# Kernel tuning notes

Measured on AMD Instinct MI355X. Metric: run time of the kernel, lower is better.

The kernel has to match this reference:

```python
import jax, jax.numpy as jnp
import numpy as np

B, CIN, COUT, L, K, HEADS, GROUPS, EPS = 16, 256, 512, 1024, 3, 8, 32, 1e-5


def group_norm(x, w, b, groups, eps=EPS):
    Bx, C, Lx = x.shape
    g = x.reshape(Bx, groups, C // groups, Lx)
    mu = g.mean(axis=(2, 3), keepdims=True)
    var = g.var(axis=(2, 3), keepdims=True)
    g = (g - mu) * jax.lax.rsqrt(var + eps)
    return g.reshape(Bx, C, Lx) * w[None, :, None] + b[None, :, None]


def conv1d(x, w, b, pad):
    y = jax.lax.conv_general_dilated(x, w, window_strides=(1,), padding=[(pad, pad)],
                                     dimension_numbers=('NCH', 'OIH', 'NCH'))
    return y + b[None, :, None]


def setup_inputs() -> dict:
    key = jax.random.key(0)
    ks = jax.random.split(key, 12)
    def kn(k, shape, fan_in, scale=1.0):
        return (np.sqrt(1.0 / fan_in) * jax.random.normal(k, shape, dtype=jnp.float32)) * scale
    return {
        'x': jax.random.normal(ks[0], (B, CIN, L), dtype=jnp.float32),
        'norm0_w': jnp.ones((CIN,), jnp.float32), 'norm0_b': jnp.zeros((CIN,), jnp.float32),
        'conv0_w': kn(ks[1], (COUT, CIN, K), CIN * K), 'conv0_b': jnp.zeros((COUT,), jnp.float32),
        'norm1_w': jnp.ones((COUT,), jnp.float32), 'norm1_b': jnp.zeros((COUT,), jnp.float32),
        'conv1_w': kn(ks[2], (COUT, COUT, K), COUT * K, 1e-5), 'conv1_b': jnp.zeros((COUT,), jnp.float32),
        'skip_w': kn(ks[3], (COUT, CIN, 1), CIN), 'skip_b': jnp.zeros((COUT,), jnp.float32),
        'norm2_w': jnp.ones((COUT,), jnp.float32), 'norm2_b': jnp.zeros((COUT,), jnp.float32),
        'qkv_w': kn(ks[4], (COUT * 3, COUT, 1), COUT), 'qkv_b': jnp.zeros((COUT * 3,), jnp.float32),
        'proj_w': kn(ks[5], (COUT, COUT, 1), COUT, 1e-5), 'proj_b': jnp.zeros((COUT,), jnp.float32),
    }


def reference(x, norm0_w, norm0_b, conv0_w, conv0_b, norm1_w, norm1_b, conv1_w, conv1_b,
              skip_w, skip_b, norm2_w, norm2_b, qkv_w, qkv_b, proj_w, proj_b):
    orig = x
    h = conv1d(jax.nn.silu(group_norm(x, norm0_w, norm0_b, min(GROUPS, CIN))), conv0_w, conv0_b, (K - 1) // 2)
    h = jax.nn.silu(group_norm(h, norm1_w, norm1_b, min(GROUPS, COUT)))
    h = conv1d(h, conv1_w, conv1_b, (K - 1) // 2)
    h = h + conv1d(orig, skip_w, skip_b, 0)  # skip (in != out), dropout p=0
    # skip_scale = 1
    # attention: qkv [B, 3C, L] -> [B*H, C/H, 3, L] (channel axis splits as H, C/H, 3)
    qkv = conv1d(group_norm(h, norm2_w, norm2_b, min(GROUPS, COUT)), qkv_w, qkv_b, 0)
    ch = COUT // HEADS
    qkv = qkv.reshape(B * HEADS, ch, 3, L)
    q, k, v = qkv[:, :, 0], qkv[:, :, 1], qkv[:, :, 2]  # each [BH, ch, L]
    scores = jnp.einsum('nci,ncj->nij', q, k) / np.sqrt(ch).astype(np.float32)
    attn = jax.nn.softmax(scores, axis=-1)
    a = jnp.einsum('nij,ncj->nci', attn, v).reshape(B, COUT, L)
    return h + conv1d(a, proj_w, proj_b, 0)
```

## Files before the change

### kernel.cpp

```cpp
#include <hip/hip_runtime.h>


typedef float f32x4 __attribute__((ext_vector_type(4)));
typedef float f32x16 __attribute__((ext_vector_type(16)));
typedef short short8 __attribute__((ext_vector_type(8)));

__device__ __forceinline__ unsigned short f2bf(float f) {
  union { float f; unsigned u; } v; v.f = f;
  return (unsigned short)((v.u + 0x7FFFu + ((v.u >> 16) & 1u)) >> 16);
}
__device__ __forceinline__ float bf2f(unsigned short h) {
  union { unsigned u; float f; } v; v.u = ((unsigned)h) << 16;
  return v.f;
}

__device__ __forceinline__ float fexp2(float x) {
  float r;
  asm("v_exp_f32 %0, %1" : "=v"(r) : "v"(x));
  return r;
}

__device__ __forceinline__ void gload_lds16(const void* g, void* l) {
  __builtin_amdgcn_global_load_lds(
      (const __attribute__((address_space(1))) unsigned int*)g,
      (__attribute__((address_space(3))) unsigned int*)l, 16, 0, 0);
}

__device__ __forceinline__ float swap_add(float x) {
  float a = x, b = x;
  asm("v_permlane32_swap_b32 %0, %1" : "+v"(a), "+v"(b));
  return a + b;
}

__device__ __forceinline__ short8 pack8(float a0, float a1, float a2, float a3,
                                        float a4, float a5, float a6, float a7) {
  unsigned x0, x1, x2, x3;
  asm("v_cvt_pk_bf16_f32 %0, %1, %2" : "=v"(x0) : "v"(a0), "v"(a1));
  asm("v_cvt_pk_bf16_f32 %0, %1, %2" : "=v"(x1) : "v"(a2), "v"(a3));
  asm("v_cvt_pk_bf16_f32 %0, %1, %2" : "=v"(x2) : "v"(a4), "v"(a5));
  asm("v_cvt_pk_bf16_f32 %0, %1, %2" : "=v"(x3) : "v"(a6), "v"(a7));
  asm("v_permlane32_swap_b32 %0, %1" : "+v"(x0), "+v"(x2));
  asm("v_permlane32_swap_b32 %0, %1" : "+v"(x1), "+v"(x3));
  union { unsigned u[4]; short8 s; } r;
  r.u[0] = x0; r.u[1] = x1; r.u[2] = x2; r.u[3] = x3;
  return r.s;
}
#define PACK8(V, B) pack8(V[B+0], V[B+1], V[B+2], V[B+3], V[B+4], V[B+5], V[B+6], V[B+7])

__global__ __launch_bounds__(256) void prep_stats(
    const float* __restrict__ c0w, const float* __restrict__ c1w,
    const float* __restrict__ skw, const float* __restrict__ qw,
    const float* __restrict__ pw,
    unsigned short* __restrict__ WT0, unsigned short* __restrict__ WT1,
    unsigned short* __restrict__ WSK, unsigned short* __restrict__ WQ,
    unsigned short* __restrict__ WP,
    const float* __restrict__ x, float2* __restrict__ mr,
    unsigned short* __restrict__ outT) {
  __shared__ float2 red[4];
  const int t = threadIdx.x;
  if (blockIdx.x >= 9216) {
    const int blk = blockIdx.x - 9216;
    const int g = blk & 31;
    const int bb = blk >> 5;
    const size_t base = ((size_t)bb * 256 + g * 8) * 1024;
    float s = 0.f, ss = 0.f;
#pragma unroll
    for (int i = t * 4; i < 8192; i += 1024) {
      const float4 v = *(const float4*)(x + base + i);
      s += (v.x + v.y) + (v.z + v.w);
      ss += (v.x * v.x + v.y * v.y) + (v.z * v.z + v.w * v.w);
    }
#pragma unroll
    for (int off = 32; off; off >>= 1) {
      s += __shfl_down(s, off);
      ss += __shfl_down(ss, off);
    }
    if ((t & 63) == 0) red[t >> 6] = make_float2(s, ss);
    __syncthreads();
    const float2 r0 = red[0], r1 = red[1], r2 = red[2], r3 = red[3];
    const float tots = (r0.x + r1.x) + (r2.x + r3.x);
    const float totss = (r0.y + r1.y) + (r2.y + r3.y);
    const float mean = tots * (1.f / 8192.f);
    const float var = totss * (1.f / 8192.f) - mean * mean;
    if (t == 0) mr[bb * 32 + g] = make_float2(mean, rsqrtf(var + 1e-5f));
    unsigned short* ob = outT + (size_t)bb * 1026 * 256 + g * 8;
    if (t < 8) {
      ob[t] = 0;
      ob[(size_t)1025 * 256 + t] = 0;
    }
    return;
  }
  int idx = blockIdx.x * 256 + t;
  if (idx < 393216) {
    const int ci = idx & 255; const int rem = idx >> 8;
    const int co = rem & 511; const int kk = rem >> 9;
    WT0[idx] = f2bf(c0w[((size_t)co * 256 + ci) * 3 + kk]); return;
  }
  idx -= 393216;
  if (idx < 786432) {
    const int ci = idx & 511; const int rem = idx >> 9;
    const int co = rem & 511; const int kk = rem >> 9;
    WT1[idx] = f2bf(c1w[((size_t)co * 512 + ci) * 3 + kk]); return;
  }
  idx -= 786432;
  if (idx < 131072) { WSK[idx] = f2bf(skw[idx]); return; }
  idx -= 131072;
  if (idx < 786432) {
    const int ci = idx & 511; const int m = idx >> 9;
    const int s = m >> 9, rem = m & 511, h = rem >> 6, c = rem & 63;
    WQ[idx] = f2bf(qw[((size_t)(h * 192 + c * 3 + s) * 512) + ci]); return;
  }
  idx -= 786432;
  WP[idx] = f2bf(pw[idx]);
}

template<int MODE, bool SILU, int C, bool PADZ, bool RAW, bool IN16>
__global__ __launch_bounds__(256) void nt_kernel(
    const float* __restrict__ in, const float2* __restrict__ st,
    const float* __restrict__ gw, const float* __restrict__ gb,
    unsigned short* __restrict__ outT, unsigned short* __restrict__ rawT) {
  constexpr int CPG = C / 32;
  __shared__ float ls[64][65];
  __shared__ unsigned short lsr[RAW ? 64 : 1][72];
  __shared__ float2 gstat[4];
  const int b = blockIdx.z, c0 = blockIdx.y * 64, l0 = blockIdx.x * 64;
  const int t = threadIdx.x;
  if (MODE == 2) {
    if (t < 4) {
      const int g = (c0 >> 4) + t;
      const float2* p = st + (((size_t)b * 4 + (g >> 3)) * 8 + (g & 7)) * 8;
      float s = 0.f, ss = 0.f;
#pragma unroll
      for (int i = 0; i < 8; ++i) { s += p[i].x; ss += p[i].y; }
      const float mean = s * (1.f / 16384.f);
      const float var = ss * (1.f / 16384.f) - mean * mean;
      gstat[t] = make_float2(mean, rsqrtf(var + 1e-5f));
    }
    __syncthreads();
  }
  const int lw = (t & 15) * 4;
  const int cr = t >> 4;
#pragma unroll
  for (int p = 0; p < 4; ++p) {
    const int c = p * 16 + cr;
    const int cc = c0 + c;
    float sc = 1.f, bi = 0.f;
    if (MODE == 1) {
      const float2 ms = st[b * 32 + cc / CPG];
      sc = gw[cc] * ms.y;
      bi = gb[cc] - ms.x * sc;
    } else if (MODE == 2) {
      const float2 ms = gstat[c >> 4];
      sc = gw[cc] * ms.y;
      bi = gb[cc] - ms.x * sc;
    }
    float4 v;
    if (IN16) {
      const ushort4 u4 = *(const ushort4*)((const unsigned short*)in +
                                           ((size_t)b * C + cc) * 1024 + l0 + lw);
      v = make_float4(bf2f(u4.x), bf2f(u4.y), bf2f(u4.z), bf2f(u4.w));
    } else {
      v = *(const float4*)(in + ((size_t)b * C + cc) * 1024 + l0 + lw);
    }
    if (RAW) {
      lsr[c][lw + 0] = f2bf(v.x);
      lsr[c][lw + 1] = f2bf(v.y);
      lsr[c][lw + 2] = f2bf(v.z);
      lsr[c][lw + 3] = f2bf(v.w);
    }
    float o[4] = {v.x * sc + bi, v.y * sc + bi, v.z * sc + bi, v.w * sc + bi};
    if (SILU) {
#pragma unroll
      for (int d = 0; d < 4; ++d) o[d] = o[d] / (1.f + __expf(-o[d]));
    }
#pragma unroll
    for (int d = 0; d < 4; ++d) ls[c][lw + d] = o[d];
  }
  __syncthreads();
  const int l = t >> 2, c16 = (t & 3) * 16;
  short8 v0, v1;
#pragma unroll
  for (int j = 0; j < 8; ++j) v0[j] = (short)f2bf(ls[c16 + j][l]);
#pragma unroll
  for (int j = 0; j < 8; ++j) v1[j] = (short)f2bf(ls[c16 + 8 + j][l]);
  unsigned short* ob = outT + ((size_t)b * 1026 + l0 + l + 1) * C + c0 + c16;
  *(short8*)ob = v0;
  *(short8*)(ob + 8) = v1;
  if (RAW) {
    short8 w0, w1;
#pragma unroll
    for (int j = 0; j < 8; ++j) w0[j] = (short)lsr[c16 + j][l];
#pragma unroll
    for (int j = 0; j < 8; ++j) w1[j] = (short)lsr[c16 + 8 + j][l];
    unsigned short* rb = rawT + ((size_t)b * 1026 + l0 + l + 1) * C + c0 + c16;
    *(short8*)rb = w0;
    *(short8*)(rb + 8) = w1;
  }
  if (PADZ) {
    const short8 z = {};
    if (blockIdx.x == 0 && t < 8)
      *(short8*)(outT + (size_t)b * 1026 * C + c0 + t * 8) = z;
    if (blockIdx.x == 15 && t < 8)
      *(short8*)(outT + ((size_t)b * 1026 + 1025) * C + c0 + t * 8) = z;
  }
}

__global__ __launch_bounds__(256) void ntE_kernel(
    const unsigned short* __restrict__ Ht, const float2* __restrict__ part,
    const float* __restrict__ gw, const float* __restrict__ gb,
    unsigned short* __restrict__ outT) {
  __shared__ float2 gstat[32];
  const int b = blockIdx.y;
  const int t = threadIdx.x;
  if (t < 32) {
    const float2* p = part + (((size_t)b * 4 + (t >> 3)) * 8 + (t & 7)) * 8;
    float s = 0.f, ss = 0.f;
#pragma unroll
    for (int i = 0; i < 8; ++i) { s += p[i].x; ss += p[i].y; }
    const float mean = s * (1.f / 16384.f);
    const float var = ss * (1.f / 16384.f) - mean * mean;
    gstat[t] = make_float2(mean, rsqrtf(var + 1e-5f));
  }
  __syncthreads();
  const int c8 = t & 63;
  const float2 ms = gstat[c8 >> 1];
  const int cbase = c8 * 8;
  const float4 g0 = *(const float4*)(gw + cbase);
  const float4 g1 = *(const float4*)(gw + cbase + 4);
  const float4 b0 = *(const float4*)(gb + cbase);
  const float4 b1 = *(const float4*)(gb + cbase + 4);
  float sc[8], bi[8];
  sc[0] = g0.x * ms.y; sc[1] = g0.y * ms.y; sc[2] = g0.z * ms.y; sc[3] = g0.w * ms.y;
  sc[4] = g1.x * ms.y; sc[5] = g1.y * ms.y; sc[6] = g1.z * ms.y; sc[7] = g1.w * ms.y;
  bi[0] = b0.x - ms.x * sc[0]; bi[1] = b0.y - ms.x * sc[1];
  bi[2] = b0.z - ms.x * sc[2]; bi[3] = b0.w - ms.x * sc[3];
  bi[4] = b1.x - ms.x * sc[4]; bi[5] = b1.y - ms.x * sc[5];
  bi[6] = b1.z - ms.x * sc[6]; bi[7] = b1.w - ms.x * sc[7];
#pragma unroll
  for (int pass = 0; pass < 4; ++pass) {
    const int lp = blockIdx.x * 16 + pass * 4 + (t >> 6) + 1;
    const size_t o = ((size_t)b * 1026 + lp) * 512 + cbase;
    const short8 v = *(const short8*)(Ht + o);
    short8 r;
#pragma unroll
    for (int e = 0; e < 8; ++e) {
      const float y = bf2f((unsigned short)v[e]) * sc[e] + bi[e];
      r[e] = (short)f2bf(y / (1.f + __expf(-y)));
    }
    *(short8*)(outT + o) = r;
  }
  const short8 z = {};
  if (blockIdx.x == 0 && t < 64)
    *(short8*)(outT + (size_t)b * 1026 * 512 + t * 8) = z;
  if (blockIdx.x == 63 && t < 64)
    *(short8*)(outT + ((size_t)b * 1026 + 1025) * 512 + t * 8) = z;
}

template<int K, bool ADD, bool SCATTER, bool FUSE, bool STATS, bool TROUT,
         bool OUT16, bool ADD16>
__global__ __launch_bounds__(256, 2) void convmm_kernel(
    const unsigned short* __restrict__ Xt, const unsigned short* __restrict__ Wt,
    const float* __restrict__ bias, const float* __restrict__ addsrc,
    float* __restrict__ outp,
    unsigned short* __restrict__ qd, unsigned short* __restrict__ kd,
    unsigned short* __restrict__ vd, int Cin, int Cout,
    const unsigned short* __restrict__ X2, const unsigned short* __restrict__ W2,
    const float* __restrict__ bias2, int Cin2, float2* __restrict__ part) {
  constexpr int XR = (K == 3) ? 160 : 128;
  __shared__ __align__(16) unsigned short smem[K * 128 * 64 + XR * 64];
  unsigned short* wT = smem;
  unsigned short* xT = smem + K * 128 * 64;
  const int t = threadIdx.x, lane = t & 63, w = t >> 6;
  const int b = blockIdx.z, co0 = blockIdx.y * 128, l0 = blockIdx.x * 128;
  const int m0 = (w >> 1) * 64, n0 = (w & 1) * 64;
  const int START = (K == 3) ? l0 : (l0 + 1);
  f32x4 acc[4][4] = {};
  for (int ci0 = 0; ci0 < Cin; ci0 += 64) {
    __syncthreads();
    for (int rr = 0; rr < K * 4; ++rr) {
      const int row = rr * 32 + (t >> 3);
      const int co = row & 127;
      const int c16 = (t & 7) ^ (co & 7);
      gload_lds16(Wt + ((size_t)(row >> 7) * Cout + co0 + co) * Cin + ci0 + c16 * 8,
                  (char*)wT + (rr * 256 + t) * 16);
    }
    for (int rr = 0; rr < XR / 32; ++rr) {
      const int r = rr * 32 + (t >> 3);
      int lp = START + r;
      if (lp > 1025) lp = 1025;
      const int c16 = (t & 7) ^ (r & 7);
      gload_lds16(Xt + ((size_t)b * 1026 + lp) * Cin + ci0 + c16 * 8,
                  (char*)xT + (rr * 256 + t) * 16);
    }
    __syncthreads();
#pragma unroll
    for (int kk = 0; kk < K; ++kk) {
#pragma unroll
      for (int ks = 0; ks < 2; ++ks) {
        short8 af[4], bfr[4];
#pragma unroll
        for (int mf = 0; mf < 4; ++mf) {
          const int row = m0 + mf * 16 + (lane & 15);
          const int u = (kk * 128 + row) * 8 + ((ks * 4 + (lane >> 4)) ^ (row & 7));
          af[mf] = *(const short8*)(wT + u * 8);
        }
#pragma unroll
        for (int nf = 0; nf < 4; ++nf) {
          const int r = n0 + nf * 16 + (lane & 15) + kk;
          const int u = r * 8 + ((ks * 4 + (lane >> 4)) ^ (r & 7));
          bfr[nf] = *(const short8*)(xT + u * 8);
        }
#pragma unroll
        for (int mf = 0; mf < 4; ++mf)
#pragma unroll
          for (int nf = 0; nf < 4; ++nf)
            acc[mf][nf] = __builtin_amdgcn_mfma_f32_16x16x32_bf16(
                af[mf], bfr[nf], acc[mf][nf], 0, 0, 0);
      }
    }
  }
  if (FUSE) {
    for (int ci0 = 0; ci0 < Cin2; ci0 += 64) {
      __syncthreads();
      for (int rr = 0; rr < 4; ++rr) {
        const int co = rr * 32 + (t >> 3);
        const int c16 = (t & 7) ^ (co & 7);
        gload_lds16(W2 + (size_t)(co0 + co) * Cin2 + ci0 + c16 * 8,
                    (char*)wT + (rr * 256 + t) * 16);
      }
      for (int rr = 0; rr < 4; ++rr) {
        const int r = rr * 32 + (t >> 3);
        const int lp = l0 + 1 + r;
        const int c16 = (t & 7) ^ (r & 7);
        gload_lds16(X2 + ((size_t)b * 1026 + lp) * Cin2 + ci0 + c16 * 8,
                    (char*)xT + (rr * 256 + t) * 16);
      }
      __syncthreads();
#pragma unroll
      for (int ks = 0; ks < 2; ++ks) {
        short8 af[4], bfr[4];
#pragma unroll
        for (int mf = 0; mf < 4; ++mf) {
          const int row = m0 + mf * 16 + (lane & 15);
          const int u = row * 8 + ((ks * 4 + (lane >> 4)) ^ (row & 7));
          af[mf] = *(const short8*)(wT + u * 8);
        }
#pragma unroll
        for (int nf = 0; nf < 4; ++nf) {
          const int r = n0 + nf * 16 + (lane & 15);
          const int u = r * 8 + ((ks * 4 + (lane >> 4)) ^ (r & 7));
          bfr[nf] = *(const short8*)(xT + u * 8);
        }
#pragma unroll
        for (int mf = 0; mf < 4; ++mf)
#pragma unroll
          for (int nf = 0; nf < 4; ++nf)
            acc[mf][nf] = __builtin_amdgcn_mfma_f32_16x16x32_bf16(
                af[mf], bfr[nf], acc[mf][nf], 0, 0, 0);
      }
    }
  }
  if (TROUT) {
    __syncthreads();
    unsigned short* TP = smem;
    float2* sr = (float2*)(TP + 128 * 128);
    float sg[4] = {}, ssg[4] = {};
#pragma unroll
    for (int mf = 0; mf < 4; ++mf)
#pragma unroll
      for (int r = 0; r < 4; ++r) {
        const int mloc = m0 + mf * 16 + (lane >> 4) * 4 + r;
        const float bv = bias[co0 + mloc];
#pragma unroll
        for (int nf = 0; nf < 4; ++nf) {
          const int l = n0 + nf * 16 + (lane & 15);
          const float v = acc[mf][nf][r] + bv;
          sg[mf] += v; ssg[mf] += v * v;
          const int u = l * 16 + ((mloc >> 3) ^ (l & 7));
          TP[u * 8 + (mloc & 7)] = f2bf(v);
        }
      }
#pragma unroll
    for (int mf = 0; mf < 4; ++mf) {
      float s = sg[mf], ss = ssg[mf];
#pragma unroll
      for (int off = 32; off; off >>= 1) {
        s += __shfl_down(s, off);
        ss += __shfl_down(ss, off);
      }
      if (lane == 0)
        sr[(((w >> 1) * 4 + mf) << 1) | (w & 1)] = make_float2(s, ss);
    }
    __syncthreads();
    for (int it = 0; it < 8; ++it) {
      const int idx = it * 256 + t;
      const int l = idx >> 4, mu = idx & 15;
      const short8 v = *(const short8*)(TP + (l * 16 + (mu ^ (l & 7))) * 8);
      *(short8*)(qd + ((size_t)b * 1026 + l0 + l + 1) * 512 + co0 + mu * 8) = v;
    }
    if (t < 8) {
      const float2 a = sr[t * 2], c = sr[t * 2 + 1];
      part[(((size_t)b * 4 + blockIdx.y) * 8 + t) * 8 + blockIdx.x] =
          make_float2(a.x + c.x, a.y + c.y);
    }
  } else if (!SCATTER) {
    float sg[4] = {}, ssg[4] = {};
#pragma unroll
    for (int mf = 0; mf < 4; ++mf) {
#pragma unroll
      for (int r = 0; r < 4; ++r) {
        const int co = co0 + m0 + mf * 16 + (lane >> 4) * 4 + r;
        float bv = bias[co];
        if (FUSE) bv += bias2[co];
#pragma unroll
        for (int nf = 0; nf < 4; ++nf) {
          const int l = l0 + n0 + nf * 16 + (lane & 15);
          const size_t o = ((size_t)b * Cout + co) * 1024 + l;
          float v = acc[mf][nf][r] + bv;
          if (ADD) {
            if (ADD16) v += bf2f(((const unsigned short*)addsrc)[o]);
            else       v += addsrc[o];
          }
          if (OUT16) ((unsigned short*)outp)[o] = f2bf(v);
          else       outp[o] = v;
          if (STATS) { sg[mf] += v; ssg[mf] += v * v; }
        }
      }
    }
    if (STATS) {
      __syncthreads();
      float2* sr = (float2*)smem;
#pragma unroll
      for (int mf = 0; mf < 4; ++mf) {
        float s = sg[mf], ss = ssg[mf];
#pragma unroll
        for (int off = 32; off; off >>= 1) {
          s += __shfl_down(s, off);
          ss += __shfl_down(ss, off);
        }
        if (lane == 0)
          sr[(((w >> 1) * 4 + mf) << 1) | (w & 1)] = make_float2(s, ss);
      }
      __syncthreads();
      if (t < 8) {
        const float2 a = sr[t * 2], c = sr[t * 2 + 1];
        part[(((size_t)b * 4 + blockIdx.y) * 8 + t) * 8 + blockIdx.x] =
            make_float2(a.x + c.x, a.y + c.y);
      }
    }
  } else {
    __syncthreads();
    unsigned short* TP = smem;
    const int sidx = co0 >> 9;
    const int mbase = co0 & 511;
    const float qscale = (sidx == 0) ? 0.18033688f : 1.0f;
    if (sidx < 2) {
#pragma unroll
      for (int mf = 0; mf < 4; ++mf)
#pragma unroll
        for (int r = 0; r < 4; ++r) {
          const int mloc = m0 + mf * 16 + (lane >> 4) * 4 + r;
          const int mg = mbase + mloc;
          const float bv = bias[(mg >> 6) * 192 + (mg & 63) * 3 + sidx];
#pragma unroll
          for (int nf = 0; nf < 4; ++nf) {
            const int l = n0 + nf * 16 + (lane & 15);
            const int u = l * 16 + ((mloc >> 3) ^ (l & 7));
            TP[u * 8 + (mloc & 7)] = f2bf((acc[mf][nf][r] + bv) * qscale);
          }
        }
      __syncthreads();
      unsigned short* dst = (sidx == 0) ? qd : kd;
      for (int it = 0; it < 8; ++it) {
        const int idx = it * 256 + t;
        const int l = idx >> 4, mu = idx & 15;
        const int mg = mbase + mu * 8;
        const int bh = b * 8 + (mg >> 6);
        const short8 v = *(const short8*)(TP + (l * 16 + (mu ^ (l & 7))) * 8);
        *(short8*)(dst + ((size_t)bh * 1024 + l0 + l) * 64 + (mg & 63)) = v;
      }
    } else {
#pragma unroll
      for (int mf = 0; mf < 4; ++mf)
#pragma unroll
        for (int r = 0; r < 4; ++r) {
          const int mloc = m0 + mf * 16 + (lane >> 4) * 4 + r;
          const int mg = mbase + mloc;
          const float bv = bias[(mg >> 6) * 192 + (mg & 63) * 3 + 2];
#pragma unroll
          for (int nf = 0; nf < 4; ++nf) {
            const int l = n0 + nf * 16 + (lane & 15);
            const int u = mloc * 16 + ((l >> 3) ^ ((mloc & 7) << 1));
            TP[u * 8 + (l & 7)] = f2bf(acc[mf][nf][r] + bv);
          }
        }
      __syncthreads();
      for (int it = 0; it < 8; ++it) {
        const int idx = it * 256 + t;
        const int mloc = idx >> 4, lu = idx & 15;
        const int mg = mbase + mloc;
        const int bh = b * 8 + (mg >> 6);
        const short8 v =
            *(const short8*)(TP + (mloc * 16 + (lu ^ ((mloc & 7) << 1))) * 8);
        *(short8*)(vd + ((size_t)bh * 64 + (mg & 63)) * 1024 + l0 + lu * 8) = v;
      }
    }
  }
}

__global__ __launch_bounds__(256, 4) void attn_mfma(
    const unsigned short* __restrict__ Qb, const unsigned short* __restrict__ Kb,
    const unsigned short* __restrict__ Vb, unsigned short* __restrict__ Ab) {
  __shared__ __align__(16) unsigned short Ks[2][64 * 64];
  __shared__ __align__(16) unsigned short Vs[2][64 * 64];
  unsigned short* QP = &Ks[0][0];
  const int t = threadIdx.x, lane = t & 63, w = t >> 6;
  const int hi = lane >> 5, l31 = lane & 31;
  const int id = blockIdx.x;
  const int slot = id >> 3;
  const int bh = ((id & 7) << 4) | (slot >> 3);
  const int b = bh >> 3, h = bh & 7;
  const int iq0 = (slot & 7) * 128;
  const unsigned short* Qg = Qb + ((size_t)bh * 1024 + iq0) * 64;
  const unsigned short* Kg = Kb + (size_t)bh * 1024 * 64;
  const unsigned short* Vg = Vb + (size_t)bh * 64 * 1024;
  for (int rr = 0; rr < 4; ++rr) {
    const int r = rr * 32 + (t >> 3), c16 = (t & 7) ^ (r & 7);
    gload_lds16(Qg + (size_t)r * 64 + c16 * 8, (char*)QP + (rr * 256 + t) * 16);
  }
  __syncthreads();
  const int irow = w * 32 + l31;
  short8 qf[4];
#pragma unroll
  for (int kc = 0; kc < 4; ++kc) {
    const int u = irow * 8 + ((kc * 2 + hi) ^ (irow & 7));
    qf[kc] = *(const short8*)(QP + u * 8);
  }
  __syncthreads();
  for (int rr = 0; rr < 2; ++rr) {
    const int r = rr * 32 + (t >> 3), c16 = (t & 7) ^ (r & 7);
    gload_lds16(Kg + (size_t)r * 64 + c16 * 8, (char*)Ks[0] + (rr * 256 + t) * 16);
    gload_lds16(Vg + (size_t)r * 1024 + c16 * 8, (char*)Vs[0] + (rr * 256 + t) * 16);
  }
  __syncthreads();
  float lsum = 0.f;
  f32x16 oA[2] = {};
  auto kv_iter = [&](const int ti, const int cur) {
    if (ti < 15) {
      const int j1 = (ti + 1) * 64;
      for (int rr = 0; rr < 2; ++rr) {
        const int r = rr * 32 + (t >> 3), c16 = (t & 7) ^ (r & 7);
        gload_lds16(Kg + (size_t)(j1 + r) * 64 + c16 * 8,
                    (char*)Ks[cur ^ 1] + (rr * 256 + t) * 16);
        gload_lds16(Vg + (size_t)r * 1024 + j1 + c16 * 8,
                    (char*)Vs[cur ^ 1] + (rr * 256 + t) * 16);
      }
    }
    f32x16 sA0 = {}, sA1 = {};
    __builtin_amdgcn_s_setprio(1);
#pragma unroll
    for (int kc = 0; kc < 4; ++kc) {
      const int r0 = l31, r1 = 32 + l31;
      const short8 k0 = *(const short8*)(Ks[cur] + (r0 * 8 + ((kc * 2 + hi) ^ (r0 & 7))) * 8);
      const short8 k1 = *(const short8*)(Ks[cur] + (r1 * 8 + ((kc * 2 + hi) ^ (r1 & 7))) * 8);
      sA0 = __builtin_amdgcn_mfma_f32_32x32x16_bf16(k0, qf[kc], sA0, 0, 0, 0);
      sA1 = __builtin_amdgcn_mfma_f32_32x32x16_bf16(k1, qf[kc], sA1, 0, 0, 0);
    }
    __builtin_amdgcn_s_setprio(0);
    float p0 = 0.f, p1 = 0.f, p2 = 0.f, p3 = 0.f;
#pragma unroll
    for (int r = 0; r < 16; r += 4) {
      sA0[r + 0] = fexp2(sA0[r + 0]); p0 += sA0[r + 0];
      sA0[r + 1] = fexp2(sA0[r + 1]); p1 += sA0[r + 1];
      sA0[r + 2] = fexp2(sA0[r + 2]); p2 += sA0[r + 2];
      sA0[r + 3] = fexp2(sA0[r + 3]); p3 += sA0[r + 3];
    }
#pragma unroll
    for (int r = 0; r < 16; r += 4) {
      sA1[r + 0] = fexp2(sA1[r + 0]); p0 += sA1[r + 0];
      sA1[r + 1] = fexp2(sA1[r + 1]); p1 += sA1[r + 1];
      sA1[r + 2] = fexp2(sA1[r + 2]); p2 += sA1[r + 2];
      sA1[r + 3] = fexp2(sA1[r + 3]); p3 += sA1[r + 3];
    }
    lsum += (p0 + p1) + (p2 + p3);
    short8 pb[4];
    pb[0] = PACK8(sA0, 0);
    pb[1] = PACK8(sA0, 8);
    pb[2] = PACK8(sA1, 0);
    pb[3] = PACK8(sA1, 8);
    __builtin_amdgcn_s_setprio(1);
#pragma unroll
    for (int cf = 0; cf < 2; ++cf) {
      const int row = cf * 32 + l31;
#pragma unroll
      for (int s = 0; s < 4; ++s) {
        const int u = row * 8 + ((s * 2 + hi) ^ (row & 7));
        const short8 va = *(const short8*)(Vs[cur] + u * 8);
        oA[cf] = __builtin_amdgcn_mfma_f32_32x32x16_bf16(va, pb[s], oA[cf], 0, 0, 0);
      }
    }
    __builtin_amdgcn_s_setprio(0);
    __syncthreads();
  };
  for (int ti = 0; ti < 16; ti += 2) {
    kv_iter(ti, 0);
    kv_iter(ti + 1, 1);
  }
  const float inv = 1.f / swap_add(lsum);
#pragma unroll
  for (int cf = 0; cf < 2; ++cf)
#pragma unroll
    for (int r = 0; r < 16; ++r) {
      const int c = cf * 32 + (r & 3) + 8 * (r >> 2) + 4 * hi;
      const int u = irow * 8 + ((c >> 3) ^ (irow & 7));
      QP[u * 8 + (c & 7)] = f2bf(oA[cf][r] * inv);
    }
  for (int rr = 0; rr < 4; ++rr) {
    const int row = w * 32 + rr * 8 + (lane >> 3);
    const int c16 = lane & 7;
    const int u = row * 8 + (c16 ^ (row & 7));
    const short8 vv = *(const short8*)(QP + u * 8);
    *(short8*)(Ab + ((size_t)b * 1026 + iq0 + row + 1) * 512 + h * 64 + c16 * 8) = vv;
  }
}

#define MB(x) ((size_t)(x) << 20)

extern "C" void kernel_launch(void* const* d_in, const int* in_sizes, int n_in,
                              void* d_out, int out_size, void* d_ws,
                              size_t ws_size, hipStream_t stream) {
  const float* x   = (const float*)d_in[0];
  const float* n0w = (const float*)d_in[1];
  const float* n0b = (const float*)d_in[2];
  const float* c0w = (const float*)d_in[3];
  const float* c0b = (const float*)d_in[4];
  const float* n1w = (const float*)d_in[5];
  const float* n1b = (const float*)d_in[6];
  const float* c1w = (const float*)d_in[7];
  const float* c1b = (const float*)d_in[8];
  const float* skw = (const float*)d_in[9];
  const float* skb = (const float*)d_in[10];
  const float* n2w = (const float*)d_in[11];
  const float* n2b = (const float*)d_in[12];
  const float* qw  = (const float*)d_in[13];
  const float* qb  = (const float*)d_in[14];
  const float* pw  = (const float*)d_in[15];
  const float* pb  = (const float*)d_in[16];
  char* wsb = (char*)d_ws;
  unsigned short* WT0 = (unsigned short*)(wsb);
  unsigned short* WT1 = (unsigned short*)(wsb + MB(1));
  unsigned short* WSK = (unsigned short*)(wsb + MB(3));
  unsigned short* WQ  = (unsigned short*)(wsb + MB(4));
  unsigned short* WP  = (unsigned short*)(wsb + MB(6));
  unsigned short* H2b = (unsigned short*)(wsb + MB(7));
  unsigned short* Qb2 = (unsigned short*)(wsb + MB(41));
  unsigned short* Kb2 = (unsigned short*)(wsb + MB(58));
  unsigned short* H0t = (unsigned short*)(wsb + MB(75));
  unsigned short* Vb2 = (unsigned short*)(wsb + MB(75));
  unsigned short* Xt2 = (unsigned short*)(wsb + MB(92));
  unsigned short* Xt0 = (unsigned short*)(wsb + MB(109));
  unsigned short* Xt1 = (unsigned short*)(wsb + MB(109));
  unsigned short* Ab  = (unsigned short*)(wsb + MB(109));
  unsigned short* Xbf = (unsigned short*)(wsb + MB(126));
  float2* MR0   = (float2*)(wsb + MB(135));
  float2* PART1 = (float2*)(wsb + MB(135) + 8192);
  float2* PART2 = (float2*)(wsb + MB(135) + 32768);
  float* outp = (float*)d_out;

  prep_stats<<<9728, 256, 0, stream>>>(c0w, c1w, skw, qw, pw,
                                       WT0, WT1, WSK, WQ, WP, x, MR0, Xt0);
  nt_kernel<1, true, 256, false, true, false><<<dim3(16, 4, 16), 256, 0, stream>>>(
      x, MR0, n0w, n0b, Xt0, Xbf);
  convmm_kernel<3, false, false, false, true, true, false, false>
      <<<dim3(8, 4, 16), 256, 0, stream>>>(
      Xt0, WT0, c0b, nullptr, nullptr, H0t, nullptr, nullptr, 256, 512,
      nullptr, nullptr, nullptr, 0, PART1);
  ntE_kernel<<<dim3(64, 16), 256, 0, stream>>>(H0t, PART1, n1w, n1b, Xt1);
  convmm_kernel<3, false, false, true, true, false, true, false>
      <<<dim3(8, 4, 16), 256, 0, stream>>>(
      Xt1, WT1, c1b, nullptr, (float*)H2b, nullptr, nullptr, nullptr, 512, 512,
      Xbf, WSK, skb, 256, PART2);
  nt_kernel<2, false, 512, false, false, true><<<dim3(16, 8, 16), 256, 0, stream>>>(
      (const float*)H2b, PART2, n2w, n2b, Xt2, nullptr);
  convmm_kernel<1, false, true, false, false, false, false, false>
      <<<dim3(8, 12, 16), 256, 0, stream>>>(
      Xt2, WQ, qb, nullptr, nullptr, Qb2, Kb2, Vb2, 512, 1536,
      nullptr, nullptr, nullptr, 0, nullptr);
  attn_mfma<<<dim3(1024), 256, 0, stream>>>(Qb2, Kb2, Vb2, Ab);
  convmm_kernel<1, true, false, false, false, false, false, true>
      <<<dim3(8, 4, 16), 256, 0, stream>>>(
      Ab, WP, pb, (const float*)H2b, outp, nullptr, nullptr, nullptr, 512, 512,
      nullptr, nullptr, nullptr, 0, nullptr);
}
```

Baseline: 182.3 us.

## Double query rows per attention block to reuse K/V tiles across two fragments

```diff
diff --git a/kernel.cpp b/kernel.cpp
--- a/kernel.cpp
+++ b/kernel.cpp
@@ -508,7 +508,7 @@
   }
 }
 
-__global__ __launch_bounds__(256, 4) void attn_mfma(
+__global__ __launch_bounds__(256, 2) void attn_mfma(
     const unsigned short* __restrict__ Qb, const unsigned short* __restrict__ Kb,
     const unsigned short* __restrict__ Vb, unsigned short* __restrict__ Ab) {
   __shared__ __align__(16) unsigned short Ks[2][64 * 64];
@@ -517,24 +517,27 @@
   const int t = threadIdx.x, lane = t & 63, w = t >> 6;
   const int hi = lane >> 5, l31 = lane & 31;
   const int id = blockIdx.x;
-  const int slot = id >> 3;
-  const int bh = ((id & 7) << 4) | (slot >> 3);
+  const int xcd = id & 7, local = id >> 3;
+  const int bh = (xcd << 4) | (local >> 2);
   const int b = bh >> 3, h = bh & 7;
-  const int iq0 = (slot & 7) * 128;
+  const int iq0 = (local & 3) * 256;
   const unsigned short* Qg = Qb + ((size_t)bh * 1024 + iq0) * 64;
   const unsigned short* Kg = Kb + (size_t)bh * 1024 * 64;
   const unsigned short* Vg = Vb + (size_t)bh * 64 * 1024;
-  for (int rr = 0; rr < 4; ++rr) {
+  for (int rr = 0; rr < 8; ++rr) {
     const int r = rr * 32 + (t >> 3), c16 = (t & 7) ^ (r & 7);
     gload_lds16(Qg + (size_t)r * 64 + c16 * 8, (char*)QP + (rr * 256 + t) * 16);
   }
   __syncthreads();
-  const int irow = w * 32 + l31;
-  short8 qf[4];
+  const int irow0 = w * 64 + l31;
+  const int irow1 = w * 64 + 32 + l31;
+  short8 qf[2][4];
 #pragma unroll
   for (int kc = 0; kc < 4; ++kc) {
-    const int u = irow * 8 + ((kc * 2 + hi) ^ (irow & 7));
-    qf[kc] = *(const short8*)(QP + u * 8);
+    const int u0 = irow0 * 8 + ((kc * 2 + hi) ^ (irow0 & 7));
+    const int u1 = irow1 * 8 + ((kc * 2 + hi) ^ (irow1 & 7));
+    qf[0][kc] = *(const short8*)(QP + u0 * 8);
+    qf[1][kc] = *(const short8*)(QP + u1 * 8);
   }
   __syncthreads();
   for (int rr = 0; rr < 2; ++rr) {
@@ -543,8 +546,8 @@
     gload_lds16(Vg + (size_t)r * 1024 + c16 * 8, (char*)Vs[0] + (rr * 256 + t) * 16);
   }
   __syncthreads();
-  float lsum = 0.f;
-  f32x16 oA[2] = {};
+  float ls0 = 0.f, ls1 = 0.f;
+  f32x16 oA[2][2] = {};
   auto kv_iter = [&](const int ti, const int cur) {
     if (ti < 15) {
       const int j1 = (ti + 1) * 64;
@@ -556,38 +559,56 @@
                     (char*)Vs[cur ^ 1] + (rr * 256 + t) * 16);
       }
     }
-    f32x16 sA0 = {}, sA1 = {};
+    f32x16 s00 = {}, s01 = {}, s10 = {}, s11 = {};
     __builtin_amdgcn_s_setprio(1);
 #pragma unroll
     for (int kc = 0; kc < 4; ++kc) {
       const int r0 = l31, r1 = 32 + l31;
       const short8 k0 = *(const short8*)(Ks[cur] + (r0 * 8 + ((kc * 2 + hi) ^ (r0 & 7))) * 8);
       const short8 k1 = *(const short8*)(Ks[cur] + (r1 * 8 + ((kc * 2 + hi) ^ (r1 & 7))) * 8);
-      sA0 = __builtin_amdgcn_mfma_f32_32x32x16_bf16(k0, qf[kc], sA0, 0, 0, 0);
-      sA1 = __builtin_amdgcn_mfma_f32_32x32x16_bf16(k1, qf[kc], sA1, 0, 0, 0);
+      s00 = __builtin_amdgcn_mfma_f32_32x32x16_bf16(k0, qf[0][kc], s00, 0, 0, 0);
+      s01 = __builtin_amdgcn_mfma_f32_32x32x16_bf16(k1, qf[0][kc], s01, 0, 0, 0);
+      s10 = __builtin_amdgcn_mfma_f32_32x32x16_bf16(k0, qf[1][kc], s10, 0, 0, 0);
+      s11 = __builtin_amdgcn_mfma_f32_32x32x16_bf16(k1, qf[1][kc], s11, 0, 0, 0);
     }
     __builtin_amdgcn_s_setprio(0);
-    float p0 = 0.f, p1 = 0.f, p2 = 0.f, p3 = 0.f;
-#pragma unroll
-    for (int r = 0; r < 16; r += 4) {
-      sA0[r + 0] = fexp2(sA0[r + 0]); p0 += sA0[r + 0];
-      sA0[r + 1] = fexp2(sA0[r + 1]); p1 += sA0[r + 1];
-      sA0[r + 2] = fexp2(sA0[r + 2]); p2 += sA0[r + 2];
-      sA0[r + 3] = fexp2(sA0[r + 3]); p3 += sA0[r + 3];
-    }
-#pragma unroll
-    for (int r = 0; r < 16; r += 4) {
-      sA1[r + 0] = fexp2(sA1[r + 0]); p0 += sA1[r + 0];
-      sA1[r + 1] = fexp2(sA1[r + 1]); p1 += sA1[r + 1];
-      sA1[r + 2] = fexp2(sA1[r + 2]); p2 += sA1[r + 2];
-      sA1[r + 3] = fexp2(sA1[r + 3]); p3 += sA1[r + 3];
-    }
-    lsum += (p0 + p1) + (p2 + p3);
-    short8 pb[4];
-    pb[0] = PACK8(sA0, 0);
-    pb[1] = PACK8(sA0, 8);
-    pb[2] = PACK8(sA1, 0);
-    pb[3] = PACK8(sA1, 8);
+    short8 pb0[4], pb1[4];
+    {
+      float p0 = 0.f, p1 = 0.f, p2 = 0.f, p3 = 0.f;
+#pragma unroll
+      for (int r = 0; r < 16; ++r) { s00[r] = fexp2(s00[r]); }
+#pragma unroll
+      for (int r = 0; r < 16; r += 4) {
+        p0 += s00[r + 0]; p1 += s00[r + 1]; p2 += s00[r + 2]; p3 += s00[r + 3];
+      }
+#pragma unroll
+      for (int r = 0; r < 16; ++r) { s01[r] = fexp2(s01[r]); }
+#pragma unroll
+      for (int r = 0; r < 16; r += 4) {
+        p0 += s01[r + 0]; p1 += s01[r + 1]; p2 += s01[r + 2]; p3 += s01[r + 3];
+      }
+      ls0 += (p0 + p1) + (p2 + p3);
+      pb0[0] = PACK8(s00, 0); pb0[1] = PACK8(s00, 8);
+      pb0[2] = PACK8(s01, 0); pb0[3] = PACK8(s01, 8);
+    }
+    {
+      float p0 = 0.f, p1 = 0.f, p2 = 0.f, p3 = 0.f;
+#pragma unroll
+      for (int r = 0; r < 16; ++r) { s10[r] = fexp2(s10[r]); }
+#pragma unroll
+      for (int r = 0; r < 16; r += 4) {
+        p0 += s10[r + 0]; p1 += s10[r + 1]; p2 += s10[r + 2]; p3 += s10[r + 3];
+      }
+#pragma unroll
+      for (int r = 0; r < 16; ++r) { s11[r] = fexp2(s11[r]); }
+#pragma unroll
+      for (int r = 0; r < 16; r += 4) {
+        p0 += s11[r + 0]; p1 += s11[r + 1]; p2 += s11[r + 2]; p3 += s11[r + 3];
+      }
+      ls1 += (p0 + p1) + (p2 + p3);
+      pb1[0] = PACK8(s10, 0); pb1[1] = PACK8(s10, 8);
+      pb1[2] = PACK8(s11, 0); pb1[3] = PACK8(s11, 8);
+    }
     __builtin_amdgcn_s_setprio(1);
 #pragma unroll
     for (int cf = 0; cf < 2; ++cf) {
@@ -596,7 +617,8 @@
       for (int s = 0; s < 4; ++s) {
         const int u = row * 8 + ((s * 2 + hi) ^ (row & 7));
         const short8 va = *(const short8*)(Vs[cur] + u * 8);
-        oA[cf] = __builtin_amdgcn_mfma_f32_32x32x16_bf16(va, pb[s], oA[cf], 0, 0, 0);
+        oA[0][cf] = __builtin_amdgcn_mfma_f32_32x32x16_bf16(va, pb0[s], oA[0][cf], 0, 0, 0);
+        oA[1][cf] = __builtin_amdgcn_mfma_f32_32x32x16_bf16(va, pb1[s], oA[1][cf], 0, 0, 0);
       }
     }
     __builtin_amdgcn_s_setprio(0);
@@ -606,17 +628,23 @@
     kv_iter(ti, 0);
     kv_iter(ti + 1, 1);
   }
-  const float inv = 1.f / swap_add(lsum);
-#pragma unroll
-  for (int cf = 0; cf < 2; ++cf)
-#pragma unroll
-    for (int r = 0; r < 16; ++r) {
-      const int c = cf * 32 + (r & 3) + 8 * (r >> 2) + 4 * hi;
-      const int u = irow * 8 + ((c >> 3) ^ (irow & 7));
-      QP[u * 8 + (c & 7)] = f2bf(oA[cf][r] * inv);
-    }
-  for (int rr = 0; rr < 4; ++rr) {
-    const int row = w * 32 + rr * 8 + (lane >> 3);
+  const float inv0 = 1.f / swap_add(ls0);
+  const float inv1 = 1.f / swap_add(ls1);
+#pragma unroll
+  for (int f = 0; f < 2; ++f) {
+    const int irow = f ? irow1 : irow0;
+    const float inv = f ? inv1 : inv0;
+#pragma unroll
+    for (int cf = 0; cf < 2; ++cf)
+#pragma unroll
+      for (int r = 0; r < 16; ++r) {
+        const int c = cf * 32 + (r & 3) + 8 * (r >> 2) + 4 * hi;
+        const int u = irow * 8 + ((c >> 3) ^ (irow & 7));
+        QP[u * 8 + (c & 7)] = f2bf(oA[f][cf][r] * inv);
+      }
+  }
+  for (int rr = 0; rr < 8; ++rr) {
+    const int row = w * 64 + rr * 8 + (lane >> 3);
     const int c16 = lane & 7;
     const int u = row * 8 + (c16 ^ (row & 7));
     const short8 vv = *(const short8*)(QP + u * 8);
@@ -686,7 +714,7 @@
       <<<dim3(8, 12, 16), 256, 0, stream>>>(
       Xt2, WQ, qb, nullptr, nullptr, Qb2, Kb2, Vb2, 512, 1536,
       nullptr, nullptr, nullptr, 0, nullptr);
-  attn_mfma<<<dim3(1024), 256, 0, stream>>>(Qb2, Kb2, Vb2, Ab);
+  attn_mfma<<<dim3(512), 256, 0, stream>>>(Qb2, Kb2, Vb2, Ab);
   convmm_kernel<1, true, false, false, false, false, false, true>
       <<<dim3(8, 4, 16), 256, 0, stream>>>(
       Ab, WP, pb, (const float*)H2b, outp, nullptr, nullptr, nullptr, 512, 512,
```

After: 176.3 us (median of 3 runs). -3.3%, faster.
